# Kernel tuning notes

Hardware: AMD Instinct MI355X
Metric: run time of the kernel (lower is better)

The kernel has to match this reference:

```python
import jax, jax.numpy as jnp
import numpy as np

B, S, D = 4, 2048, 1024
H, DK, DV = 16, 64, 64


def setup_inputs() -> dict:
    key = jax.random.key(0)
    ks = jax.random.split(key, 9)
    std = 1.0 / np.sqrt(D)
    inp = {
        "x": jax.random.normal(ks[0], (B, S, D), jnp.float32),
        "c": jax.random.normal(ks[1], (B, S, D), jnp.float32),
        "Wq_x": jax.random.normal(ks[2], (D, H * DK), jnp.float32) * std,
        "Wk_x": jax.random.normal(ks[3], (D, H * DK), jnp.float32) * std,
        "Wv_x": jax.random.normal(ks[4], (D, H * DV), jnp.float32) * std,
        "Wq_c": jax.random.normal(ks[5], (D, H * DK), jnp.float32) * std,
        "Wk_c": jax.random.normal(ks[6], (D, H * DK), jnp.float32) * std,
        "Wv_c": jax.random.normal(ks[7], (D, H * DV), jnp.float32) * std,
        "W_proj": jax.random.normal(ks[8], (2 * H * DV, D), jnp.float32) * (1.0 / np.sqrt(2 * H * DV)),
        "b_proj": jnp.zeros((D,), jnp.float32),
    }
    return inp


def _heads(t, hd):
    # [B,S,H*hd] -> [B,H,S,hd]
    b, s, _ = t.shape
    return t.reshape(b, s, H, hd).transpose(0, 2, 1, 3)


def reference(x, c, Wq_x, Wk_x, Wv_x, Wq_c, Wk_c, Wv_c, W_proj, b_proj):
    q = jnp.concatenate([_heads(x @ Wq_x, DK), _heads(c @ Wq_c, DK)], axis=-1)  # [B,H,S,2DK]
    k = jnp.concatenate([_heads(x @ Wk_x, DK), _heads(c @ Wk_c, DK)], axis=-1)
    v = jnp.concatenate([_heads(x @ Wv_x, DV), _heads(c @ Wv_c, DV)], axis=-1)  # [B,H,S,2DV]
    # NOTE: original scales by sqrt(k_dim), not sqrt(2*k_dim) (faithful)
    scores = jnp.einsum("bhqd,bhkd->bhqk", q, k) / np.float32(np.sqrt(DK))
    attn = jax.nn.softmax(scores, axis=-1)
    out = jnp.einsum("bhqk,bhkd->bhqd", attn, v)  # [B,H,S,2DV]
    out = out.transpose(0, 2, 1, 3).reshape(x.shape[0], x.shape[1], -1)  # [B,S,H*2DV]
    return out @ W_proj + b_proj
```

## Files before the change

kernel.cpp:

```cpp
#include <hip/hip_runtime.h>
#include <hip/hip_bf16.h>
#include <stdint.h>

#define BB 4
#define SS 2048
#define DD 1024
#define HH 16
#define DHH 128

typedef __bf16 bf16x8 __attribute__((ext_vector_type(8)));
typedef __bf16 bf16x4 __attribute__((ext_vector_type(4)));
typedef float  f32x4  __attribute__((ext_vector_type(4)));

#define SL2E 0.180336880111186f

#if __has_builtin(__builtin_amdgcn_exp2f)
#define EXP2(x) __builtin_amdgcn_exp2f(x)
#else
#define EXP2(x) exp2f(x)
#endif

#define GLOAD_LDS16(gp, lp) \
  __builtin_amdgcn_global_load_lds((const __attribute__((address_space(1))) unsigned int*)(gp), \
                                   (__attribute__((address_space(3))) unsigned int*)(lp), 16, 0, 0)

#define SBAR() do { asm volatile("" ::: "memory"); \
                    __builtin_amdgcn_s_barrier();  \
                    asm volatile("" ::: "memory"); } while (0)

#define MFMA_BF16(a, b, c) __builtin_amdgcn_mfma_f32_16x16x32_bf16((a), (b), (c), 0, 0, 0)

__global__ void cast2_kernel(const float* __restrict__ x, const float* __restrict__ c,
                             __bf16* __restrict__ out, int n) {
    int i = (blockIdx.x * blockDim.x + threadIdx.x) * 4;
    const float* src = (i < n) ? (x + i) : (c + (i - n));
    f32x4 v = *(const f32x4*)src;
    bf16x4 o;
    o[0] = (__bf16)v[0]; o[1] = (__bf16)v[1]; o[2] = (__bf16)v[2]; o[3] = (__bf16)v[3];
    *(bf16x4*)(out + i) = o;
}

__global__ void transpose_cast_kernel(const float* __restrict__ in, __bf16* __restrict__ out,
                                      int K, int N) {
    __shared__ float tile[32][33];
    int n0 = blockIdx.x * 32, k0 = blockIdx.y * 32;
    int tx = threadIdx.x, ty = threadIdx.y;
    #pragma unroll
    for (int i = 0; i < 32; i += 8)
        tile[ty + i][tx] = in[(size_t)(k0 + ty + i) * N + n0 + tx];
    __syncthreads();
    #pragma unroll
    for (int i = 0; i < 32; i += 8)
        out[(size_t)(n0 + ty + i) * K + k0 + tx] = (__bf16)tile[tx][ty + i];
}

__global__ void transpose6_kernel(const float* s0, const float* s1, const float* s2,
                                  const float* s3, const float* s4, const float* s5,
                                  __bf16* __restrict__ dst) {
    const float* srcs[6] = {s0, s1, s2, s3, s4, s5};
    const float* __restrict__ in = srcs[blockIdx.z];
    __bf16* __restrict__ out = dst + (size_t)blockIdx.z * 1024 * 1024;
    __shared__ float tile[32][33];
    int n0 = blockIdx.x * 32, k0 = blockIdx.y * 32;
    int tx = threadIdx.x, ty = threadIdx.y;
    #pragma unroll
    for (int i = 0; i < 32; i += 8)
        tile[ty + i][tx] = in[(size_t)(k0 + ty + i) * 1024 + n0 + tx];
    __syncthreads();
    #pragma unroll
    for (int i = 0; i < 32; i += 8)
        out[(size_t)(n0 + ty + i) * 1024 + k0 + tx] = (__bf16)tile[tx][ty + i];
}

template <int EPI>
__global__ __launch_bounds__(512, 2)
void gemm256_kernel(const __bf16* __restrict__ A0, const __bf16* __restrict__ A1,
                    const __bf16* __restrict__ B0, const __bf16* __restrict__ B1,
                    int K, void* __restrict__ outp, const float* __restrict__ bias) {
    const int z = blockIdx.z;
    const __bf16* __restrict__ A  = z ? A1 : A0;
    const __bf16* __restrict__ Bt = z ? B1 : B0;
    const int qkv_off = z * 64;

    __shared__ __align__(16) char smem[131072];

    const int tid = threadIdx.x;
    const int wave = tid >> 6, lane = tid & 63;
    const int l15 = lane & 15, quad = lane >> 4;
    const int wr = wave >> 2, wc = wave & 3;

    const int gx = gridDim.x;
    const int nwg = gx * gridDim.y;
    const int hwl = blockIdx.y * gx + blockIdx.x;
    const int lg  = (hwl & 7) * (nwg >> 3) + (hwl >> 3);
    const int m0 = (lg % gx) * 256, n0 = (lg / gx) * 256;

    const int rA = tid >> 2;
    const int cs = (tid & 3) ^ ((tid >> 4) & 3);
    const __bf16* aS0 = A  + (size_t)(m0 + rA) * K + cs * 8;
    const __bf16* aS1 = aS0 + (size_t)128 * K;
    const __bf16* bS0 = Bt + (size_t)(n0 + rA) * K + cs * 8;
    const __bf16* bS1 = bS0 + (size_t)128 * K;
    const int ldsA = wave * 1024;
    const int ldsB = 16384 + wave * 1024;

    const int swz = ((quad ^ (l15 >> 2)) & 3) * 16;
    const int ra = (wr * 128 + l15) * 64 + swz;
    const int rb = 16384 + (wc * 64 + l15) * 64 + swz;

    f32x4 acc[8][4] = {};
    bf16x8 afc[2][4], bfc[2][4], afB[4];
    const int NT = K >> 5;

    #define STAGE_A(tt) do { const int bo_ = ((tt) & 3) * 32768; \
        GLOAD_LDS16(aS0 + (size_t)(tt) * 32, smem + bo_ + ldsA); \
        GLOAD_LDS16(aS1 + (size_t)(tt) * 32, smem + bo_ + ldsA + 8192); } while (0)
    #define STAGE_B(tt) do { const int bo_ = ((tt) & 3) * 32768; \
        GLOAD_LDS16(bS0 + (size_t)(tt) * 32, smem + bo_ + ldsB); \
        GLOAD_LDS16(bS1 + (size_t)(tt) * 32, smem + bo_ + ldsB + 8192); } while (0)

    STAGE_A(0); STAGE_B(0);
    STAGE_A(1); STAGE_B(1);
    STAGE_A(2); STAGE_B(2);
    asm volatile("s_waitcnt vmcnt(8)" ::: "memory");
    SBAR();
    #pragma unroll
    for (int i = 0; i < 4; ++i) afc[0][i] = *(const bf16x8*)(smem + ra + i * 1024);
    #pragma unroll
    for (int i = 0; i < 4; ++i) bfc[0][i] = *(const bf16x8*)(smem + rb + i * 1024);

    for (int tp = 0; tp < NT / 2; ++tp) {
        #pragma unroll
        for (int u = 0; u < 2; ++u) {
            const int t = 2 * tp + u;
            const int co = (t & 3) * 32768;
            const int cn = ((t + 1) & 3) * 32768;
            #pragma unroll
            for (int i = 0; i < 4; ++i)
                afB[i] = *(const bf16x8*)(smem + co + ra + (4 + i) * 1024);
            if (t + 3 < NT) STAGE_A(t + 3);
            SBAR();
            __builtin_amdgcn_s_setprio(1);
            #pragma unroll
            for (int mi = 0; mi < 4; ++mi)
                #pragma unroll
                for (int ni = 0; ni < 4; ++ni)
                    acc[mi][ni] = MFMA_BF16(afc[u][mi], bfc[u][ni], acc[mi][ni]);
            __builtin_amdgcn_s_setprio(0);
            if (t + 3 < NT) STAGE_B(t + 3);
            if (t < NT - 3)       asm volatile("s_waitcnt vmcnt(8)" ::: "memory");
            else if (t == NT - 3) asm volatile("s_waitcnt vmcnt(4)" ::: "memory");
            else if (t == NT - 2) asm volatile("s_waitcnt vmcnt(0)" ::: "memory");
            SBAR();
            #pragma unroll
            for (int i = 0; i < 4; ++i)
                afc[u ^ 1][i] = *(const bf16x8*)(smem + cn + ra + i * 1024);
            #pragma unroll
            for (int i = 0; i < 4; ++i)
                bfc[u ^ 1][i] = *(const bf16x8*)(smem + cn + rb + i * 1024);
            __builtin_amdgcn_s_setprio(1);
            #pragma unroll
            for (int mi = 0; mi < 4; ++mi)
                #pragma unroll
                for (int ni = 0; ni < 4; ++ni)
                    acc[4 + mi][ni] = MFMA_BF16(afB[mi], bfc[u][ni], acc[4 + mi][ni]);
            __builtin_amdgcn_s_setprio(0);
        }
    }
    #undef STAGE_A
    #undef STAGE_B

    const size_t nQKV = (size_t)BB * HH * SS * DHH;
    #pragma unroll
    for (int mi = 0; mi < 8; ++mi) {
        #pragma unroll
        for (int ni = 0; ni < 4; ++ni) {
            #pragma unroll
            for (int rr = 0; rr < 4; ++rr) {
                int m = m0 + wr * 128 + mi * 16 + quad * 4 + rr;
                int n = n0 + wc * 64 + ni * 16 + l15;
                if (EPI == 2) {
                    int h = m >> 6, dl = m & 63;
                    int b = n >> 11, s = n & (SS - 1);
                    __bf16* vt = (__bf16*)outp;
                    vt[(((size_t)b * HH + h) * DHH + dl + qkv_off) * SS + s] = (__bf16)acc[mi][ni][rr];
                } else {
                    int b = m >> 11, s = m & (SS - 1);
                    int n1 = n & 1023;
                    int h = n1 >> 6, d = (n1 & 63) + qkv_off;
                    if (n < 1024) {
                        __bf16* q = (__bf16*)outp;
                        q[(((size_t)b * HH + h) * SS + s) * DHH + d] = (__bf16)(acc[mi][ni][rr] * SL2E);
                    } else {
                        int dsw = (((d >> 3) ^ (s & 15)) << 3) | (d & 7);
                        __bf16* kq = (__bf16*)outp + nQKV;
                        kq[(((size_t)b * HH + h) * SS + s) * DHH + dsw] = (__bf16)acc[mi][ni][rr];
                    }
                }
            }
        }
    }
}

__global__ __launch_bounds__(512, 2)
void gemm_proj_kernel(const __bf16* __restrict__ A, const __bf16* __restrict__ Bt,
                      int K, float* __restrict__ outp, const float* __restrict__ bias) {
    __shared__ __align__(16) char smem[98304];

    const int tid = threadIdx.x;
    const int wave = tid >> 6, lane = tid & 63;
    const int l15 = lane & 15, quad = lane >> 4;
    const int wr = wave >> 1, wc = wave & 1;

    const int gx = gridDim.x;
    const int nwg = gx * gridDim.y;
    const int hwl = blockIdx.y * gx + blockIdx.x;
    const int lg  = (hwl & 7) * (nwg >> 3) + (hwl >> 3);
    const int m0 = (lg % gx) * 256, n0 = (lg / gx) * 128;

    const int rA = tid >> 2;
    const int cs = (tid & 3) ^ ((tid >> 4) & 3);
    const __bf16* aS0 = A  + (size_t)(m0 + rA) * K + cs * 8;
    const __bf16* aS1 = aS0 + (size_t)128 * K;
    const __bf16* bS0 = Bt + (size_t)(n0 + rA) * K + cs * 8;
    const int ldsA = wave * 1024;
    const int ldsB = 16384 + wave * 1024;

    const int swz = ((quad ^ (l15 >> 2)) & 3) * 16;
    const int ra = (wr * 64 + l15) * 64 + swz;
    const int rb = 16384 + (wc * 64 + l15) * 64 + swz;

    f32x4 acc[4][4] = {};
    bf16x8 afc[2][4], bfc[2][4];
    const int NT = K >> 5;

    #define STAGE_P(tt) do { const int bo_ = ((tt) & 3) * 24576; \
        GLOAD_LDS16(aS0 + (size_t)(tt) * 32, smem + bo_ + ldsA); \
        GLOAD_LDS16(aS1 + (size_t)(tt) * 32, smem + bo_ + ldsA + 8192); \
        GLOAD_LDS16(bS0 + (size_t)(tt) * 32, smem + bo_ + ldsB); } while (0)

    STAGE_P(0); STAGE_P(1); STAGE_P(2);
    asm volatile("s_waitcnt vmcnt(6)" ::: "memory");
    SBAR();
    #pragma unroll
    for (int i = 0; i < 4; ++i) afc[0][i] = *(const bf16x8*)(smem + ra + i * 1024);
    #pragma unroll
    for (int i = 0; i < 4; ++i) bfc[0][i] = *(const bf16x8*)(smem + rb + i * 1024);

    for (int tp = 0; tp < NT / 2; ++tp) {
        #pragma unroll
        for (int u = 0; u < 2; ++u) {
            const int t = 2 * tp + u;
            const int cn = ((t + 1) & 3) * 24576;
            if (t + 3 < NT) STAGE_P(t + 3);
            if (t < NT - 3)       asm volatile("s_waitcnt vmcnt(6)" ::: "memory");
            else if (t == NT - 3) asm volatile("s_waitcnt vmcnt(3)" ::: "memory");
            else if (t == NT - 2) asm volatile("s_waitcnt vmcnt(0)" ::: "memory");
            SBAR();
            #pragma unroll
            for (int i = 0; i < 4; ++i)
                afc[u ^ 1][i] = *(const bf16x8*)(smem + cn + ra + i * 1024);
            #pragma unroll
            for (int i = 0; i < 4; ++i)
                bfc[u ^ 1][i] = *(const bf16x8*)(smem + cn + rb + i * 1024);
            __builtin_amdgcn_s_setprio(1);
            #pragma unroll
            for (int mi = 0; mi < 4; ++mi)
                #pragma unroll
                for (int ni = 0; ni < 4; ++ni)
                    acc[mi][ni] = MFMA_BF16(afc[u][mi], bfc[u][ni], acc[mi][ni]);
            __builtin_amdgcn_s_setprio(0);
        }
    }
    #undef STAGE_P

    #pragma unroll
    for (int mi = 0; mi < 4; ++mi)
        #pragma unroll
        for (int ni = 0; ni < 4; ++ni)
            #pragma unroll
            for (int rr = 0; rr < 4; ++rr) {
                int m = m0 + wr * 64 + mi * 16 + quad * 4 + rr;
                int n = n0 + wc * 64 + ni * 16 + l15;
                outp[(size_t)m * 1024 + n] = acc[mi][ni][rr] + bias[n];
            }
}

#define LDS_BUFSZ 32768
#define LDS_VT    16384
#define LDS_PS    65536
__global__ __launch_bounds__(256, 2)
void attn_kernel(const __bf16* __restrict__ Q, const __bf16* __restrict__ Kg,
                 const __bf16* __restrict__ Vg, __bf16* __restrict__ O) {
    __shared__ __align__(16) char smem[81920];

    const int t = threadIdx.x;
    const int wave = t >> 6, lane = t & 63;
    const int l15 = lane & 15, quad = lane >> 4;

    const int lin = blockIdx.x;
    const int mt = (lin >> 3) & 7;
    const int bh = ((lin >> 6) << 3) + (lin & 7);

    const int b = bh >> 4, h = bh & 15;
    const size_t base  = (size_t)bh * SS * DHH;
    const size_t vbase = (size_t)bh * DHH * SS;

    int kaddr[4];
    #pragma unroll
    for (int kst = 0; kst < 4; ++kst)
        kaddr[kst] = l15 * 256 + (((4 * kst + quad) ^ l15) & 15) * 16;
    int vaddr[2];
    #pragma unroll
    for (int hf = 0; hf < 2; ++hf)
        vaddr[hf] = LDS_VT + l15 * 128 + (((4 * hf + quad) ^ (l15 & 7)) & 7) * 16;
    int pwN[2];
    #pragma unroll
    for (int nl = 0; nl < 2; ++nl)
        pwN[nl] = LDS_PS + (wave * 64 + l15) * 64 +
                  (((nl * 2 + (quad >> 1)) ^ ((l15 >> 2) & 3)) & 3) * 16 + (quad & 1) * 8;
    const int par = LDS_PS + (wave * 64 + l15) * 64 + ((quad ^ (l15 >> 2)) & 3) * 16;

    const __bf16* kstage = Kg + base + (size_t)wave * 2048 + lane * 8;
    const __bf16* vstage = Vg + vbase + (size_t)(wave * 32 + (lane >> 3)) * SS
                           + ((lane & 7) ^ ((lane >> 3) & 7)) * 8;

    #define STAGE_KV(kt_, bo_) do { \
        _Pragma("unroll") \
        for (int i_ = 0; i_ < 4; ++i_) \
            GLOAD_LDS16(kstage + (size_t)(kt_) * 8192 + i_ * 512, \
                        smem + (bo_) + wave * 4096 + i_ * 1024); \
        _Pragma("unroll") \
        for (int i_ = 0; i_ < 4; ++i_) \
            GLOAD_LDS16(vstage + (kt_) * 64 + (size_t)i_ * 8 * SS, \
                        smem + (bo_) + LDS_VT + wave * 4096 + i_ * 1024); \
    } while (0)

    bf16x8 qf[4][4];
    #pragma unroll
    for (int ms = 0; ms < 4; ++ms) {
        int row = mt * 256 + wave * 64 + ms * 16 + l15;
        #pragma unroll
        for (int kst = 0; kst < 4; ++kst)
            qf[ms][kst] = *(const bf16x8*)(Q + base + (size_t)row * DHH + kst * 32 + quad * 8);
    }

    f32x4 oacc[4][8] = {};
    float li_[4] = {};

    STAGE_KV(0, 0);
    __syncthreads();

    for (int kt = 0; kt < SS / 64; ++kt) {
        const int co = (kt & 1) * LDS_BUFSZ;
        if (kt + 1 < SS / 64) STAGE_KV(kt + 1, co ^ LDS_BUFSZ);

        #pragma unroll
        for (int hf = 0; hf < 2; ++hf) {
            #pragma unroll
            for (int nl = 0; nl < 2; ++nl) {
                f32x4 sxn[4] = {};
                __builtin_amdgcn_s_setprio(1);
                #pragma unroll
                for (int kst = 0; kst < 4; ++kst) {
                    bf16x8 kf = *(const bf16x8*)(smem + co + kaddr[kst] + 8192 * hf + 4096 * nl);
                    sxn[0] = MFMA_BF16(kf, qf[0][kst], sxn[0]);
                    sxn[1] = MFMA_BF16(kf, qf[1][kst], sxn[1]);
                    sxn[2] = MFMA_BF16(kf, qf[2][kst], sxn[2]);
                    sxn[3] = MFMA_BF16(kf, qf[3][kst], sxn[3]);
                }
                __builtin_amdgcn_s_setprio(0);
                #pragma unroll
                for (int ms = 0; ms < 4; ++ms) {
                    bf16x4 pk;
                    #pragma unroll
                    for (int rr = 0; rr < 4; ++rr) {
                        float p = EXP2(sxn[ms][rr]);
                        li_[ms] += p;
                        pk[rr] = (__bf16)p;
                    }
                    *(bf16x4*)(smem + pwN[nl] + 1024 * ms) = pk;
                }
            }

            bf16x8 pa[4];
            #pragma unroll
            for (int ms = 0; ms < 4; ++ms)
                pa[ms] = *(const bf16x8*)(smem + par + 1024 * ms);
            __builtin_amdgcn_s_setprio(1);
            #pragma unroll
            for (int ds = 0; ds < 8; ++ds) {
                bf16x8 vf = *(const bf16x8*)(smem + co + vaddr[hf] + 2048 * ds);
                oacc[0][ds] = MFMA_BF16(pa[0], vf, oacc[0][ds]);
                oacc[1][ds] = MFMA_BF16(pa[1], vf, oacc[1][ds]);
                oacc[2][ds] = MFMA_BF16(pa[2], vf, oacc[2][ds]);
                oacc[3][ds] = MFMA_BF16(pa[3], vf, oacc[3][ds]);
            }
            __builtin_amdgcn_s_setprio(0);
        }
        __syncthreads();
    }
    #undef STAGE_KV

    #pragma unroll
    for (int ms = 0; ms < 4; ++ms) {
        float v = li_[ms];
        v += __shfl_xor(v, 16);
        v += __shfl_xor(v, 32);
        li_[ms] = 1.f / v;
    }

    #pragma unroll
    for (int ms = 0; ms < 4; ++ms)
        #pragma unroll
        for (int rr = 0; rr < 4; ++rr) {
            float sc = __shfl(li_[ms], (lane & 48) | (quad * 4 + rr));
            int s = mt * 256 + wave * 64 + ms * 16 + quad * 4 + rr;
            size_t ob = ((size_t)b * SS + s) * (HH * DHH) + (size_t)h * DHH;
            #pragma unroll
            for (int ds = 0; ds < 8; ++ds)
                O[ob + ds * 16 + l15] = (__bf16)(oacc[ms][ds][rr] * sc);
        }
}

extern "C" void kernel_launch(void* const* d_in, const int* in_sizes, int n_in,
                              void* d_out, int out_size, void* d_ws, size_t ws_size,
                              hipStream_t stream) {
    const float* x      = (const float*)d_in[0];
    const float* c      = (const float*)d_in[1];
    const float* Wq_x   = (const float*)d_in[2];
    const float* Wk_x   = (const float*)d_in[3];
    const float* Wv_x   = (const float*)d_in[4];
    const float* Wq_c   = (const float*)d_in[5];
    const float* Wk_c   = (const float*)d_in[6];
    const float* Wv_c   = (const float*)d_in[7];
    const float* W_proj = (const float*)d_in[8];
    const float* b_proj = (const float*)d_in[9];

    const size_t nXC  = (size_t)BB * SS * DD;
    const size_t nW   = (size_t)DD * DD;
    const size_t nWP  = (size_t)(2 * HH * 64) * DD;
    const size_t nQKV = (size_t)BB * HH * SS * DHH;

    __bf16* ws  = (__bf16*)d_ws;
    __bf16* xb  = ws;
    __bf16* cb  = xb + nXC;
    __bf16* wt0 = cb + nXC;
    __bf16* wt2 = wt0 + 2 * nW;
    __bf16* wt3 = wt0 + 3 * nW;
    __bf16* wt5 = wt0 + 5 * nW;
    __bf16* wtp = wt0 + 6 * nW;
    __bf16* Qb  = wtp + nWP;
    __bf16* Kb  = Qb + nQKV;
    __bf16* Vb  = Kb + nQKV;
    __bf16* Ob  = xb;

    cast2_kernel<<<(int)(2 * nXC / 1024), 256, 0, stream>>>(x, c, xb, (int)nXC);

    transpose6_kernel<<<dim3(32, 32, 6), dim3(32, 8), 0, stream>>>(
        Wq_x, Wk_x, Wv_x, Wq_c, Wk_c, Wv_c, wt0);
    transpose_cast_kernel<<<dim3(32, 64), dim3(32, 8), 0, stream>>>(W_proj, wtp, 2048, 1024);

    gemm256_kernel<4><<<dim3(32, 8, 2), 512, 0, stream>>>(xb, cb, wt0, wt3, 1024, Qb, nullptr);
    gemm256_kernel<2><<<dim3(4, 32, 2), 512, 0, stream>>>(wt2, wt5, xb, cb, 1024, Vb, nullptr);

    attn_kernel<<<dim3(512), 256, 0, stream>>>(Qb, Kb, Vb, Ob);

    gemm_proj_kernel<<<dim3(32, 8), 512, 0, stream>>>(Ob, wtp, 2048, (float*)d_out, b_proj);
}
```

Baseline: 454.6 us.

## Restructure QKV GEMM to K=64 double-buffered tiles with phased loads

Replaces the 4-stage K=32 pipeline in the QKV projection GEMM with a 2-stage K=64 double buffer. Each iteration is split into four phases that interleave A-row staging and fine-grained vmcnt waits with MFMA work on 32-row slices. LDS uses an 8-way XOR swizzle over 128-byte rows, and the wave-to-row mapping is interleaved. The intent is fewer barriers per unit of K and better overlap of global-to-LDS loads with compute, at the cost of shallower prefetch depth and more barriers per tile.

```diff
diff --git a/kernel.cpp b/kernel.cpp
--- a/kernel.cpp
+++ b/kernel.cpp
@@ -74,9 +74,9 @@
 
 template <int EPI>
 __global__ __launch_bounds__(512, 2)
-void gemm256_kernel(const __bf16* __restrict__ A0, const __bf16* __restrict__ A1,
-                    const __bf16* __restrict__ B0, const __bf16* __restrict__ B1,
-                    int K, void* __restrict__ outp, const float* __restrict__ bias) {
+void gemm8p_kernel(const __bf16* __restrict__ A0, const __bf16* __restrict__ A1,
+                   const __bf16* __restrict__ B0, const __bf16* __restrict__ B1,
+                   int K, void* __restrict__ outp) {
     const int z = blockIdx.z;
     const __bf16* __restrict__ A  = z ? A1 : A0;
     const __bf16* __restrict__ Bt = z ? B1 : B0;
@@ -95,80 +95,78 @@
     const int lg  = (hwl & 7) * (nwg >> 3) + (hwl >> 3);
     const int m0 = (lg % gx) * 256, n0 = (lg / gx) * 256;
 
-    const int rA = tid >> 2;
-    const int cs = (tid & 3) ^ ((tid >> 4) & 3);
-    const __bf16* aS0 = A  + (size_t)(m0 + rA) * K + cs * 8;
-    const __bf16* aS1 = aS0 + (size_t)128 * K;
-    const __bf16* bS0 = Bt + (size_t)(n0 + rA) * K + cs * 8;
-    const __bf16* bS1 = bS0 + (size_t)128 * K;
-    const int ldsA = wave * 1024;
-    const int ldsB = 16384 + wave * 1024;
-
-    const int swz = ((quad ^ (l15 >> 2)) & 3) * 16;
-    const int ra = (wr * 128 + l15) * 64 + swz;
-    const int rb = 16384 + (wc * 64 + l15) * 64 + swz;
+    const int cs = (lane & 7) ^ ((lane >> 3) & 7);
+    const __bf16* aSt = A  + (size_t)(m0 + wave * 8 + (lane >> 3)) * K + cs * 8;
+    const __bf16* bSt = Bt + (size_t)(n0 + wave * 8 + (lane >> 3)) * K + cs * 8;
+    const int ldso = wave * 1024;
+
+    const int fsw = l15 & 7;
+    const int cks0 = ((quad ^ fsw) & 7) * 16;
+    const int cks1 = (((quad + 4) ^ fsw) & 7) * 16;
+    const int ra0 = (wr * 16 + l15) * 128;
+    const int rb0 = (wc * 64 + l15) * 128;
 
     f32x4 acc[8][4] = {};
-    bf16x8 afc[2][4], bfc[2][4], afB[4];
-    const int NT = K >> 5;
-
-    #define STAGE_A(tt) do { const int bo_ = ((tt) & 3) * 32768; \
-        GLOAD_LDS16(aS0 + (size_t)(tt) * 32, smem + bo_ + ldsA); \
-        GLOAD_LDS16(aS1 + (size_t)(tt) * 32, smem + bo_ + ldsA + 8192); } while (0)
-    #define STAGE_B(tt) do { const int bo_ = ((tt) & 3) * 32768; \
-        GLOAD_LDS16(bS0 + (size_t)(tt) * 32, smem + bo_ + ldsB); \
-        GLOAD_LDS16(bS1 + (size_t)(tt) * 32, smem + bo_ + ldsB + 8192); } while (0)
-
-    STAGE_A(0); STAGE_B(0);
-    STAGE_A(1); STAGE_B(1);
-    STAGE_A(2); STAGE_B(2);
-    asm volatile("s_waitcnt vmcnt(8)" ::: "memory");
+    const int NT = K >> 6;
+
+    #define STG_A(T_, q_) GLOAD_LDS16(aSt + (size_t)(q_) * 64 * K + (T_) * 64, \
+        smem + ((T_) & 1) * 32768 + (q_) * 8192 + ldso)
+    #define STG_B(T_) do { _Pragma("unroll") \
+        for (int j_ = 0; j_ < 4; ++j_) \
+            GLOAD_LDS16(bSt + (size_t)j_ * 64 * K + (T_) * 64, \
+                smem + 65536 + ((T_) & 1) * 32768 + j_ * 8192 + ldso); } while (0)
+
+    STG_B(0);
+    STG_A(0, 0); STG_A(0, 1); STG_A(0, 2); STG_A(0, 3);
+    asm volatile("s_waitcnt vmcnt(3)" ::: "memory");
     SBAR();
-    #pragma unroll
-    for (int i = 0; i < 4; ++i) afc[0][i] = *(const bf16x8*)(smem + ra + i * 1024);
-    #pragma unroll
-    for (int i = 0; i < 4; ++i) bfc[0][i] = *(const bf16x8*)(smem + rb + i * 1024);
-
-    for (int tp = 0; tp < NT / 2; ++tp) {
-        #pragma unroll
-        for (int u = 0; u < 2; ++u) {
-            const int t = 2 * tp + u;
-            const int co = (t & 3) * 32768;
-            const int cn = ((t + 1) & 3) * 32768;
-            #pragma unroll
-            for (int i = 0; i < 4; ++i)
-                afB[i] = *(const bf16x8*)(smem + co + ra + (4 + i) * 1024);
-            if (t + 3 < NT) STAGE_A(t + 3);
+
+    for (int T = 0; T < NT; ++T) {
+        const int ca = (T & 1) * 32768;
+        const int cb = 65536 + (T & 1) * 32768;
+        const bool stg = (T + 1 < NT);
+        bf16x8 bfr[4][2];
+        #pragma unroll
+        for (int p = 0; p < 4; ++p) {
+            bf16x8 af[2][2];
+            #pragma unroll
+            for (int ml = 0; ml < 2; ++ml) {
+                af[ml][0] = *(const bf16x8*)(smem + ca + ra0 + (2 * p + ml) * 4096 + cks0);
+                af[ml][1] = *(const bf16x8*)(smem + ca + ra0 + (2 * p + ml) * 4096 + cks1);
+            }
+            if (p == 0) {
+                #pragma unroll
+                for (int ni = 0; ni < 4; ++ni) {
+                    bfr[ni][0] = *(const bf16x8*)(smem + cb + rb0 + ni * 2048 + cks0);
+                    bfr[ni][1] = *(const bf16x8*)(smem + cb + rb0 + ni * 2048 + cks1);
+                }
+            }
+            if (stg) {
+                if (p == 0) STG_B(T + 1);
+                STG_A(T + 1, p);
+            }
+            if (p == 0)      { if (stg) asm volatile("s_waitcnt vmcnt(7)" ::: "memory");
+                               else    asm volatile("s_waitcnt vmcnt(2)" ::: "memory"); }
+            else if (p == 1) { if (stg) asm volatile("s_waitcnt vmcnt(7)" ::: "memory");
+                               else    asm volatile("s_waitcnt vmcnt(1)" ::: "memory"); }
+            else if (p == 2) { if (stg) asm volatile("s_waitcnt vmcnt(7)" ::: "memory");
+                               else    asm volatile("s_waitcnt vmcnt(0)" ::: "memory"); }
+            else             { if (stg) asm volatile("s_waitcnt vmcnt(3)" ::: "memory"); }
             SBAR();
             __builtin_amdgcn_s_setprio(1);
             #pragma unroll
-            for (int mi = 0; mi < 4; ++mi)
+            for (int kk = 0; kk < 2; ++kk)
                 #pragma unroll
-                for (int ni = 0; ni < 4; ++ni)
-                    acc[mi][ni] = MFMA_BF16(afc[u][mi], bfc[u][ni], acc[mi][ni]);
+                for (int ml = 0; ml < 2; ++ml)
+                    #pragma unroll
+                    for (int ni = 0; ni < 4; ++ni)
+                        acc[2 * p + ml][ni] = MFMA_BF16(af[ml][kk], bfr[ni][kk], acc[2 * p + ml][ni]);
             __builtin_amdgcn_s_setprio(0);
-            if (t + 3 < NT) STAGE_B(t + 3);
-            if (t < NT - 3)       asm volatile("s_waitcnt vmcnt(8)" ::: "memory");
-            else if (t == NT - 3) asm volatile("s_waitcnt vmcnt(4)" ::: "memory");
-            else if (t == NT - 2) asm volatile("s_waitcnt vmcnt(0)" ::: "memory");
             SBAR();
-            #pragma unroll
-            for (int i = 0; i < 4; ++i)
-                afc[u ^ 1][i] = *(const bf16x8*)(smem + cn + ra + i * 1024);
-            #pragma unroll
-            for (int i = 0; i < 4; ++i)
-                bfc[u ^ 1][i] = *(const bf16x8*)(smem + cn + rb + i * 1024);
-            __builtin_amdgcn_s_setprio(1);
-            #pragma unroll
-            for (int mi = 0; mi < 4; ++mi)
-                #pragma unroll
-                for (int ni = 0; ni < 4; ++ni)
-                    acc[4 + mi][ni] = MFMA_BF16(afB[mi], bfc[u][ni], acc[4 + mi][ni]);
-            __builtin_amdgcn_s_setprio(0);
         }
     }
-    #undef STAGE_A
-    #undef STAGE_B
+    #undef STG_A
+    #undef STG_B
 
     const size_t nQKV = (size_t)BB * HH * SS * DHH;
     #pragma unroll
@@ -177,7 +175,7 @@
         for (int ni = 0; ni < 4; ++ni) {
             #pragma unroll
             for (int rr = 0; rr < 4; ++rr) {
-                int m = m0 + wr * 128 + mi * 16 + quad * 4 + rr;
+                int m = m0 + wr * 16 + mi * 32 + quad * 4 + rr;
                 int n = n0 + wc * 64 + ni * 16 + l15;
                 if (EPI == 2) {
                     int h = m >> 6, dl = m & 63;
@@ -461,8 +459,8 @@
         Wq_x, Wk_x, Wv_x, Wq_c, Wk_c, Wv_c, wt0);
     transpose_cast_kernel<<<dim3(32, 64), dim3(32, 8), 0, stream>>>(W_proj, wtp, 2048, 1024);
 
-    gemm256_kernel<4><<<dim3(32, 8, 2), 512, 0, stream>>>(xb, cb, wt0, wt3, 1024, Qb, nullptr);
-    gemm256_kernel<2><<<dim3(4, 32, 2), 512, 0, stream>>>(wt2, wt5, xb, cb, 1024, Vb, nullptr);
+    gemm8p_kernel<4><<<dim3(32, 8, 2), 512, 0, stream>>>(xb, cb, wt0, wt3, 1024, Qb);
+    gemm8p_kernel<2><<<dim3(4, 32, 2), 512, 0, stream>>>(wt2, wt5, xb, cb, 1024, Vb);
 
     attn_kernel<<<dim3(512), 256, 0, stream>>>(Qb, Kb, Vb, Ob);
 
```

New measurement: 447.1 us. Within noise of the previous version (-1.7%).
